# Optimization experiments

Hardware: AMD Instinct MI355X
Metric: run time of the kernel (lower is better)

## Reference

```python
import jax, jax.numpy as jnp
import numpy as np
import math

B, N, NDIM = 8, 8192, 2
WIDTH, HEADS, OUT_C, LATENT_D = 128, 4, 128, 128
N_POINT, N_SAMPLE, RADIUS, PATCH = 128, 8, 0.2, 8
MAX_DEG = 15
POS_DIM = NDIM * (1 + 2 * MAX_DEG)  # 62
SELF_LAYERS = 3


def setup_inputs() -> dict:
    ks = jax.random.split(jax.random.key(0), 16)
    f32 = jnp.float32
    def nrm(k, shape, s=0.02):
        return jax.random.normal(k, shape, dtype=f32) * s
    W = WIDTH
    inp = {
        'points': jax.random.uniform(ks[0], (B, N, NDIM), dtype=f32),
        'pe_w': nrm(ks[1], (POS_DIM, W)), 'pe_b': jnp.zeros((W,), f32),
        'conv1_w': nrm(ks[2], (W, W + NDIM, PATCH, 1)), 'conv1_b': jnp.zeros((W,), f32),
        'conv2_w': nrm(ks[3], (W, W, PATCH, 1)), 'conv2_b': jnp.zeros((W,), f32),
        'output_tokens': jax.random.normal(ks[4], (LATENT_D, W), dtype=f32),
        'ln_pre_s': jnp.ones((W,), f32), 'ln_pre_b': jnp.zeros((W,), f32),
        'c_ln1_s': jnp.ones((W,), f32), 'c_ln1_b': jnp.zeros((W,), f32),
        'c_ln2_s': jnp.ones((W,), f32), 'c_ln2_b': jnp.zeros((W,), f32),
        'c_q_w': nrm(ks[5], (W, W)), 'c_q_b': jnp.zeros((W,), f32),
        'c_kv_w': nrm(ks[6], (W, 2 * W)), 'c_kv_b': jnp.zeros((2 * W,), f32),
        'c_proj_w': nrm(ks[7], (W, W)), 'c_proj_b': jnp.zeros((W,), f32),
        'c_ln3_s': jnp.ones((W,), f32), 'c_ln3_b': jnp.zeros((W,), f32),
        'c_mlp1_w': nrm(ks[8], (W, 4 * W)), 'c_mlp1_b': jnp.zeros((4 * W,), f32),
        'c_mlp2_w': nrm(ks[9], (4 * W, W)), 'c_mlp2_b': jnp.zeros((W,), f32),
        's_ln1_s': jnp.ones((SELF_LAYERS, W), f32), 's_ln1_b': jnp.zeros((SELF_LAYERS, W), f32),
        's_qkv_w': nrm(ks[10], (SELF_LAYERS, W, 3 * W)), 's_qkv_b': jnp.zeros((SELF_LAYERS, 3 * W), f32),
        's_proj_w': nrm(ks[11], (SELF_LAYERS, W, W)), 's_proj_b': jnp.zeros((SELF_LAYERS, W), f32),
        's_ln2_s': jnp.ones((SELF_LAYERS, W), f32), 's_ln2_b': jnp.zeros((SELF_LAYERS, W), f32),
        's_mlp1_w': nrm(ks[12], (SELF_LAYERS, W, 4 * W)), 's_mlp1_b': jnp.zeros((SELF_LAYERS, 4 * W), f32),
        's_mlp2_w': nrm(ks[13], (SELF_LAYERS, 4 * W, W)), 's_mlp2_b': jnp.zeros((SELF_LAYERS, W), f32),
        'ln_post_s': jnp.ones((W,), f32), 'ln_post_b': jnp.zeros((W,), f32),
        'out_w': nrm(ks[14], (W, OUT_C)), 'out_b': jnp.zeros((OUT_C,), f32),
    }
    return inp


def _layer_norm(x, s, b):
    m = jnp.mean(x, -1, keepdims=True)
    v = jnp.mean(jnp.square(x - m), -1, keepdims=True)
    return (x - m) * jax.lax.rsqrt(v + 1e-5) * s + b


def _posenc_nerf(x):
    # point-e nerf posenc: concat([x, sin(xb), sin(xb + pi/2)])
    scales = 2.0 ** jnp.arange(MAX_DEG, dtype=jnp.float32)
    xb = (x[..., None, :] * scales[:, None]).reshape(*x.shape[:-1], -1)
    emb = jnp.sin(jnp.concatenate([xb, xb + 0.5 * jnp.pi], axis=-1))
    return jnp.concatenate([x, emb], axis=-1)  # [..., C*(1+2*MAX_DEG)]


def _mha(q, k, v):
    b, tq, w = q.shape
    dh = w // HEADS
    qh = q.reshape(b, tq, HEADS, dh)
    kh = k.reshape(b, -1, HEADS, dh)
    vh = v.reshape(b, -1, HEADS, dh)
    scores = jnp.einsum('bqhd,bkhd->bhqk', qh, kh) * (1.0 / math.sqrt(dh))
    attn = jax.nn.softmax(scores, axis=-1)
    return jnp.einsum('bhqk,bkhd->bqhd', attn, vh).reshape(b, tq, w)


def _circ_conv(x, w, b):
    # Conv2d kernel (PATCH,1), stride 1, circular padding (PATCH//2, 0)
    p = PATCH // 2
    xp = jnp.concatenate([x[:, :, -p:], x, x[:, :, :p]], axis=2)
    y = jax.lax.conv_general_dilated(xp, w, (1, 1), 'VALID',
                                     dimension_numbers=('NCHW', 'OIHW', 'NCHW'))
    return y + b[None, :, None, None]


def _forward(points, pe_w, pe_b, conv1_w, conv1_b, conv2_w, conv2_b, output_tokens,
             ln_pre_s, ln_pre_b, c_ln1_s, c_ln1_b, c_ln2_s, c_ln2_b, c_q_w, c_q_b,
             c_kv_w, c_kv_b, c_proj_w, c_proj_b, c_ln3_s, c_ln3_b, c_mlp1_w, c_mlp1_b,
             c_mlp2_w, c_mlp2_b, s_ln1_s, s_ln1_b, s_qkv_w, s_qkv_b, s_proj_w, s_proj_b,
             s_ln2_s, s_ln2_b, s_mlp1_w, s_mlp1_b, s_mlp2_w, s_mlp2_b, ln_post_s, ln_post_b,
             out_w, out_b):
    bsz, n, _ = points.shape
    dataset_emb = _posenc_nerf(points) @ pe_w + pe_b             # [B,N,W]
    # ---- PointSetEmbedding (fps_method='first' -> first n_point centers) ----
    new_xyz = points[:, :N_POINT]                                # [B,S,2]
    sqr = jnp.sum(jnp.square(new_xyz[:, :, None] - points[:, None]), -1)  # [B,S,N]
    base = jnp.broadcast_to(jnp.arange(n, dtype=jnp.int32), sqr.shape)
    idx = jnp.where(sqr > RADIUS ** 2, n, base)
    idx = jnp.sort(idx, axis=-1)[:, :, :N_SAMPLE]
    idx = jnp.where(idx == n, idx[:, :, :1], idx)                # [B,S,K] ball-query indices
    gather = jax.vmap(lambda a, i: a[i])
    grouped_xyz = gather(points, idx) - new_xyz[:, :, None]      # [B,S,K,2] relative coords
    grouped_pts = gather(dataset_emb, idx)                       # [B,S,K,W]
    feats = jnp.concatenate([grouped_xyz, grouped_pts], -1)      # [B,S,K,W+2]
    x = jnp.transpose(feats, (0, 3, 2, 1))                       # [B,C,K,S]
    x = jax.nn.silu(_circ_conv(x, conv1_w, conv1_b))
    x = jax.nn.silu(_circ_conv(x, conv2_w, conv2_b))
    data_tokens = jnp.transpose(x.mean(axis=2), (0, 2, 1))       # [B,S,W]
    # ---- Perceiver: cross-attn then self-attn ----
    lat = jnp.broadcast_to(output_tokens[None], (bsz, LATENT_D, WIDTH))
    h = _layer_norm(jnp.concatenate([data_tokens, lat], axis=1), ln_pre_s, ln_pre_b)
    q = _layer_norm(h, c_ln1_s, c_ln1_b) @ c_q_w + c_q_b
    kv = _layer_norm(dataset_emb, c_ln2_s, c_ln2_b) @ c_kv_w + c_kv_b
    k, v = jnp.split(kv, 2, axis=-1)
    h = h + (_mha(q, k, v) @ c_proj_w + c_proj_b)
    t = _layer_norm(h, c_ln3_s, c_ln3_b)
    h = h + (jax.nn.gelu(t @ c_mlp1_w + c_mlp1_b, approximate=False) @ c_mlp2_w + c_mlp2_b)
    for i in range(SELF_LAYERS):
        qkv = _layer_norm(h, s_ln1_s[i], s_ln1_b[i]) @ s_qkv_w[i] + s_qkv_b[i]
        q, k, v = jnp.split(qkv, 3, axis=-1)
        h = h + (_mha(q, k, v) @ s_proj_w[i] + s_proj_b[i])
        t = _layer_norm(h, s_ln2_s[i], s_ln2_b[i])
        h = h + (jax.nn.gelu(t @ s_mlp1_w[i] + s_mlp1_b[i], approximate=False) @ s_mlp2_w[i] + s_mlp2_b[i])
    h = h[:, -LATENT_D:]
    return jnp.tanh(_layer_norm(h, ln_post_s, ln_post_b) @ out_w + out_b)


def reference(points, pe_w, pe_b, conv1_w, conv1_b, conv2_w, conv2_b, output_tokens,
              ln_pre_s, ln_pre_b, c_ln1_s, c_ln1_b, c_ln2_s, c_ln2_b, c_q_w, c_q_b,
              c_kv_w, c_kv_b, c_proj_w, c_proj_b, c_ln3_s, c_ln3_b, c_mlp1_w, c_mlp1_b,
              c_mlp2_w, c_mlp2_b, s_ln1_s, s_ln1_b, s_qkv_w, s_qkv_b, s_proj_w, s_proj_b,
              s_ln2_s, s_ln2_b, s_mlp1_w, s_mlp1_b, s_mlp2_w, s_mlp2_b, ln_post_s, ln_post_b,
              out_w, out_b):
    return _forward(points, pe_w, pe_b, conv1_w, conv1_b, conv2_w, conv2_b, output_tokens,
                    ln_pre_s, ln_pre_b, c_ln1_s, c_ln1_b, c_ln2_s, c_ln2_b, c_q_w, c_q_b,
                    c_kv_w, c_kv_b, c_proj_w, c_proj_b, c_ln3_s, c_ln3_b, c_mlp1_w, c_mlp1_b,
                    c_mlp2_w, c_mlp2_b, s_ln1_s, s_ln1_b, s_qkv_w, s_qkv_b, s_proj_w, s_proj_b,
                    s_ln2_s, s_ln2_b, s_mlp1_w, s_mlp1_b, s_mlp2_w, s_mlp2_b, ln_post_s, ln_post_b,
                    out_w, out_b)
```

## Files before the change

### kernel.cpp

```cpp
#include <hip/hip_runtime.h>
#include <math.h>


namespace {

constexpr int NP = 8192;
constexpr int WD = 128;
constexpr int POSD = 62;
constexpr float R2C = 0.04f;
constexpr float QSCALE = 0.17677669529663687f;
constexpr float HALFPI = 1.5707963705062866f;

typedef __bf16 bf16x8 __attribute__((ext_vector_type(8)));
typedef float f32x4 __attribute__((ext_vector_type(4)));
union U16B { uint4 u; bf16x8 h; unsigned short s[8]; };

__device__ __forceinline__ float b2f(unsigned short u) {
  unsigned v = (unsigned)u << 16;
  return __builtin_bit_cast(float, v);
}

constexpr size_t AO_WQ     = 0;
constexpr size_t AO_WKV    = 16384;
constexpr size_t AO_WPROJC = 49152;
// ... 66 lines not shown
    const float* __restrict__ w1, const float* __restrict__ w2,
    unsigned short* __restrict__ dst) {
  const size_t i = (size_t)blockIdx.x * 256 + threadIdx.x;
  if (i >= AO_TOT) return;
  float v;
  if (i < AO_WKV) {
    size_t j = i;            v = wq[(j & 127) * 128 + (j >> 7)];
  } else if (i < AO_WPROJC) {
    size_t j = i - AO_WKV;   v = wkv[(j & 127) * 256 + (j >> 7)];
  } else if (i < AO_WMLP1C) {
    size_t j = i - AO_WPROJC; v = wprojc[(j & 127) * 128 + (j >> 7)];
  } else if (i < AO_WMLP2C) {
    size_t j = i - AO_WMLP1C; v = wmlp1c[(j & 127) * 512 + (j >> 7)];
  } else if (i < AO_WQKVS) {
    size_t j = i - AO_WMLP2C; v = wmlp2c[(j & 511) * 128 + (j >> 9)];
  } else if (i < AO_WPROJS) {
    size_t j = i - AO_WQKVS;
    size_t L = j / 49152, jj = j % 49152;
    v = wqkvs[L * 49152 + (jj & 127) * 384 + (jj >> 7)];
  } else if (i < AO_WMLP1S) {
    size_t j = i - AO_WPROJS;
    size_t L = j / 16384, jj = j % 16384;
    v = wprojs[L * 16384 + (jj & 127) * 128 + (jj >> 7)];
  } else if (i < AO_WMLP2S) {
    size_t j = i - AO_WMLP1S;
    size_t L = j / 65536, jj = j % 65536;
    v = wmlp1s[L * 65536 + (jj & 127) * 512 + (jj >> 7)];
  } else if (i < AO_WOUT) {
    size_t j = i - AO_WMLP2S;
    size_t L = j / 65536, jj = j % 65536;
    v = wmlp2s[L * 65536 + (jj & 511) * 128 + (jj >> 9)];
  } else if (i < AO_W1B) {
    size_t j = i - AO_WOUT;  v = wout[(j & 127) * 128 + (j >> 7)];
  } else if (i < AO_W2B) {
    size_t j = i - AO_W1B;
    size_t c = j / 1056, k = j % 1056;
    v = (k < 1040) ? w1[c * 1040 + k] : 0.f;
  } else {
    size_t j = i - AO_W2B;   v = w2[(j >> 10) * 1024 + (j & 1023)];
  }
  __bf16 bv = (__bf16)v;
  dst[i] = *(unsigned short*)&bv;
}

__global__ __launch_bounds__(256) void k_kvgc(
    const unsigned short* __restrict__ embb,
    const unsigned short* __restrict__ wkvt,
    const float* __restrict__ kvbias, unsigned short* __restrict__ kb,
    unsigned short* __restrict__ vb, const float* __restrict__ lnS,
    const float* __restrict__ lnB, const float* __restrict__ pts,
    const unsigned short* __restrict__ w1b, const float* __restrict__ b1,
    const unsigned short* __restrict__ w2b, const float* __restrict__ b2,
    float* __restrict__ dtok) {
  __shared__ __align__(16) char shl[45568];
  __shared__ int sid[2][8];
  const int bx = blockIdx.x;
  const int tid = threadIdx.x;
  const int w = tid >> 6, lane = tid & 63;
  const int l15 = lane & 15, l16 = lane >> 4;

  if (bx >= 512) {
    const int kx = bx - 512;
    const int row0 = (kx & 2047) * 32;
    const int nblk = kx >> 11;
    unsigned short (*Ab)[136] = (unsigned short(*)[136])shl;
    unsigned short (*Bt)[136] = (unsigned short(*)[136])(shl + 8704);
    {
      const int n = tid >> 1, hf = tid & 1;
      const unsigned short* src =
          wkvt + ((size_t)(nblk * 128 + n) * 128 + hf * 64);
#pragma unroll
      for (int q8 = 0; q8 < 8; ++q8)
        *(uint4*)&Bt[n][hf * 64 + q8 * 8] = *(const uint4*)(src + q8 * 8);
    }
    {
      const int r = tid >> 3, seg = tid & 7;
      const unsigned short* ap = embb + (size_t)(row0 + r) * WD + seg * 16;
      U16B w0, w1u;
      w0.u = *(const uint4*)ap;
      w1u.u = *(const uint4*)(ap + 8);
      float xv[16];
#pragma unroll
      for (int j = 0; j < 8; ++j) {
        xv[j] = b2f(w0.s[j]);
        xv[8 + j] = b2f(w1u.s[j]);
      }
      float s = 0.f, sq = 0.f;
#pragma unroll
      for (int j = 0; j < 16; ++j) { s += xv[j]; sq += xv[j] * xv[j]; }
      s += __shfl_xor(s, 1);  sq += __shfl_xor(sq, 1);
      s += __shfl_xor(s, 2);  sq += __shfl_xor(sq, 2);
      s += __shfl_xor(s, 4);  sq += __shfl_xor(sq, 4);
      const float m = s * (1.f / 128.f);
      const float var = fmaxf(sq * (1.f / 128.f) - m * m, 0.f);
      const float rinv = 1.0f / sqrtf(var + 1e-5f);
      U16B u0, u1;
#pragma unroll
      for (int j = 0; j < 16; ++j) {
        int col = seg * 16 + j;
        float y = (xv[j] - m) * rinv * lnS[col] + lnB[col];
        if (j < 8) u0.h[j] = (__bf16)y; else u1.h[j - 8] = (__bf16)y;
      }
      *(uint4*)&Ab[r][seg * 16] = u0.u;
      *(uint4*)&Ab[r][seg * 16 + 8] = u1.u;
    }
    __syncthreads();
    const int rt = w >> 1, ch = w & 1;
    f32x4 acc[4];
#pragma unroll
    for (int j = 0; j < 4; ++j) acc[j] = (f32x4){0.f, 0.f, 0.f, 0.f};
#pragma unroll
    for (int kk = 0; kk < 4; ++kk) {
      U16B ua;
      ua.u = *(const uint4*)&Ab[rt * 16 + l15][kk * 32 + l16 * 8];
#pragma unroll
      for (int ct4 = 0; ct4 < 4; ++ct4) {
        U16B ub;
        ub.u = *(const uint4*)&Bt[(ch * 4 + ct4) * 16 + l15][kk * 32 + l16 * 8];
        acc[ct4] = __builtin_amdgcn_mfma_f32_16x16x32_bf16(ua.h, ub.h,
                                                           acc[ct4], 0, 0, 0);
      }
    }
    unsigned short* Dp = (nblk == 1) ? vb : kb;
#pragma unroll
    for (int ct4 = 0; ct4 < 4; ++ct4) {
      int colL = (ch * 4 + ct4) * 16 + l15;
      float bv = kvbias[nblk * 128 + colL];
#pragma unroll
      for (int r = 0; r < 4; ++r) {
        int row = row0 + rt * 16 + l16 * 4 + r;
        __bf16 ov = (__bf16)(acc[ct4][r] + bv);
        Dp[(size_t)row * 128 + colL] = *(unsigned short*)&ov;
      }
    }
    return;
  }

  const int blk = bx;
  const int b = blk >> 6;
  const int i0 = (blk & 63) * 2;
  unsigned short* ftp  = (unsigned short*)shl;
  unsigned short* Bt1p = (unsigned short*)(shl + 4224);
  unsigned short* y1p  = (unsigned short*)shl;
  unsigned short* Bt2p = (unsigned short*)(shl + 12288);

  if (w < 2) {
    const int i = i0 + w;
    const float cx = pts[((size_t)b * NP + i) * 2];
    const float cy = pts[((size_t)b * NP + i) * 2 + 1];
    int cnt = 0;
    for (int j0 = 0; j0 < NP; j0 += 64) {
      int j = j0 + lane;
      float dx = pts[((size_t)b * NP + j) * 2] - cx;
      float dy = pts[((size_t)b * NP + j) * 2 + 1] - cy;
      float d2 = __fadd_rn(__fmul_rn(dx, dx), __fmul_rn(dy, dy));
      bool ok = !(d2 > R2C);
      unsigned long long m = __ballot(ok);
      int ord = cnt + __popcll(m & ((1ull << lane) - 1ull));
      if (ok && ord < 8) sid[w][ord] = j;
      cnt += (int)__popcll(m);
      if (cnt >= 8) break;
    }
    if (lane < 8 && lane >= cnt) sid[w][lane] = sid[w][0];
  }
  __syncthreads();
  {
    const int pr = tid >> 4, c8 = tid & 15;
    const int spx = pr >> 3, s = pr & 7;
    U16B u;
    u.u = *(const uint4*)(embb + ((size_t)b * NP + sid[spx][s]) * WD + c8 * 8);
#pragma unroll
    for (int j = 0; j < 8; ++j)
      ftp[((size_t)spx * 132 + 2 + c8 * 8 + j) * 8 + s] = u.s[j];
  }
  if (tid < 32) {
    int spx = tid >> 4, s = (tid >> 1) & 7, d = tid & 1;
    float dv = pts[((size_t)b * NP + sid[spx][s]) * 2 + d] -
               pts[((size_t)b * NP + i0 + spx) * 2 + d];
    __bf16 bv = (__bf16)dv;
    ftp[((size_t)spx * 132 + d) * 8 + s] = *(unsigned short*)&bv;
  }
  __syncthreads();
  {
    const int n = tid >> 4, g = tid & 15;
    const int pt = n >> 3, h = n & 7;
#pragma unroll
    for (int it = 0; it < 9; ++it) {
      int cin = g + it * 16;
      if (cin < 130) {
        U16B u0;
        u0.u = *(const uint4*)&ftp[((size_t)pt * 132 + cin) * 8];
        U16B u;
#pragma unroll
        for (int p = 0; p < 8; ++p) u.s[p] = u0.s[(h + p + 4) & 7];
        *(uint4*)&Bt1p[n * 1064 + cin * 8] = u.u;
      } else if (cin < 132) {
        uint4 z; z.x = z.y = z.z = z.w = 0;
        *(uint4*)&Bt1p[n * 1064 + cin * 8] = z;
      }
    }
  }
  __syncthreads();
  f32x4 acc1[2];
  acc1[0] = (f32x4){0.f, 0.f, 0.f, 0.f};
  acc1[1] = (f32x4){0.f, 0.f, 0.f, 0.f};
  {
    const unsigned short* w1r = w1b + (size_t)(w * 32 + l15) * 1056;
#pragma unroll 3
    for (int ks = 0; ks < 33; ++ks) {
      const int k0 = ks * 32 + l16 * 8;
      U16B a0, a1, bb;
      a0.u = *(const uint4*)(w1r + k0);
      a1.u = *(const uint4*)(w1r + 16 * 1056 + k0);
      bb.u = *(const uint4*)&Bt1p[l15 * 1064 + k0];
      acc1[0] = __builtin_amdgcn_mfma_f32_16x16x32_bf16(a0.h, bb.h, acc1[0],
                                                        0, 0, 0);
      acc1[1] = __builtin_amdgcn_mfma_f32_16x16x32_bf16(a1.h, bb.h, acc1[1],
                                                        0, 0, 0);
    }
  }
  __syncthreads();
  {
    const int pt = l15 >> 3, h = l15 & 7;
#pragma unroll
    for (int t = 0; t < 2; ++t)
#pragma unroll
      for (int r = 0; r < 4; ++r) {
        int c = w * 32 + t * 16 + l16 * 4 + r;
        float x = acc1[t][r] + b1[c];
        float sy = x / (1.f + __expf(-x));
        __bf16 bh = (__bf16)sy;
        unsigned short bits = *(unsigned short*)&bh;
        size_t yb = ((size_t)pt * 128 + c) * 24;
        y1p[yb + h] = bits;
        if (h == 0) y1p[yb + 8] = bits;
      }
  }
  f32x4 acc2[2][2];
#pragma unroll
  for (int t = 0; t < 2; ++t)
#pragma unroll
    for (int nt = 0; nt < 2; ++nt) acc2[t][nt] = (f32x4){0.f, 0.f, 0.f, 0.f};
  for (int hf = 0; hf < 2; ++hf) {
    __syncthreads();
    {
      const int n2 = tid >> 3, g = tid & 7;
      const int pt = n2 / 9, h2 = n2 % 9;
#pragma unroll
      for (int it = 0; it < 8; ++it) {
        int c1loc = g + it * 8;
        if (n2 < 18) {
          int c1 = hf * 64 + c1loc;
          size_t yb = ((size_t)pt * 128 + c1) * 24;
          U16B u0;
          u0.u = *(const uint4*)&y1p[yb];
          unsigned short yv[9];
#pragma unroll
          for (int j = 0; j < 8; ++j) yv[j] = u0.s[j];
          yv[8] = y1p[yb + 8];
          U16B o;
#pragma unroll
          for (int p = 0; p < 8; ++p) o.s[p] = yv[(h2 + p + 5) % 9];
          *(uint4*)&Bt2p[n2 * 520 + c1loc * 8] = o.u;
        } else {
          uint4 z; z.x = z.y = z.z = z.w = 0;
          *(uint4*)&Bt2p[n2 * 520 + c1loc * 8] = z;
        }
      }
    }
    __syncthreads();
    const unsigned short* w2r = w2b + (size_t)(w * 32 + l15) * 1024 + hf * 512;
#pragma unroll 4
    for (int ks = 0; ks < 16; ++ks) {
      const int k0 = ks * 32 + l16 * 8;
      U16B a0, a1, b0, b1u;
      a0.u = *(const uint4*)(w2r + k0);
      a1.u = *(const uint4*)(w2r + 16 * 1024 + k0);
      b0.u = *(const uint4*)&Bt2p[l15 * 520 + k0];
      b1u.u = *(const uint4*)&Bt2p[(16 + l15) * 520 + k0];
      acc2[0][0] = __builtin_amdgcn_mfma_f32_16x16x32_bf16(a0.h, b0.h,
                                                           acc2[0][0], 0, 0, 0);
      acc2[0][1] = __builtin_amdgcn_mfma_f32_16x16x32_bf16(a0.h, b1u.h,
                                                           acc2[0][1], 0, 0, 0);
      acc2[1][0] = __builtin_amdgcn_mfma_f32_16x16x32_bf16(a1.h, b0.h,
                                                           acc2[1][0], 0, 0, 0);
      acc2[1][1] = __builtin_amdgcn_mfma_f32_16x16x32_bf16(a1.h, b1u.h,
                                                           acc2[1][1], 0, 0, 0);
    }
  }
  float s0[2][4], s1[2][4];
#pragma unroll
  for (int t = 0; t < 2; ++t)
#pragma unroll
    for (int r = 0; r < 4; ++r) { s0[t][r] = 0.f; s1[t][r] = 0.f; }
#pragma unroll
  for (int t = 0; t < 2; ++t)
#pragma unroll
    for (int nt = 0; nt < 2; ++nt) {
      const int n2 = nt * 16 + l15;
      if (n2 < 18) {
        const float wgt = (n2 % 9 == 0) ? 2.f : 1.f;
#pragma unroll
        for (int r = 0; r < 4; ++r) {
          int c = w * 32 + t * 16 + l16 * 4 + r;
          float x = acc2[t][nt][r] + b2[c];
          float sv = wgt * (x / (1.f + __expf(-x)));
          if (n2 < 9) s0[t][r] += sv; else s1[t][r] += sv;
        }
      }
    }
#pragma unroll
  for (int t = 0; t < 2; ++t)
#pragma unroll
    for (int r = 0; r < 4; ++r) {
      float a = s0[t][r], bq = s1[t][r];
      a += __shfl_xor(a, 1);  bq += __shfl_xor(bq, 1);
      a += __shfl_xor(a, 2);  bq += __shfl_xor(bq, 2);
      a += __shfl_xor(a, 4);  bq += __shfl_xor(bq, 4);
      a += __shfl_xor(a, 8);  bq += __shfl_xor(bq, 8);
      if (l15 == 0) {
        int c = w * 32 + t * 16 + l16 * 4 + r;
        dtok[((size_t)b * 128 + i0) * WD + c] = a / 10.0f;
        dtok[((size_t)b * 128 + i0 + 1) * WD + c] = bq / 10.0f;
      }
    }
}

__global__ __launch_bounds__(64) void k_concat_ln(
    const float* __restrict__ dtok, const float* __restrict__ otok,
    const float* __restrict__ g, const float* __restrict__ bta,
    float* __restrict__ h0) {
  const int row = blockIdx.x;
  const int b = row >> 8, t = row & 255;
  const int lane = threadIdx.x;
  const float* src = (t < 128) ? (dtok + ((size_t)b * 128 + t) * WD)
                               : (otok + (size_t)(t - 128) * WD);
  const float2 x2 = *(const float2*)(src + lane * 2);
  float s = x2.x + x2.y;
  float sq = x2.x * x2.x + x2.y * x2.y;
#pragma unroll
  for (int o = 1; o < 64; o <<= 1) {
    s += __shfl_xor(s, o);
    sq += __shfl_xor(sq, o);
  }
  float m = s * (1.f / 128.f);
  float var = fmaxf(sq * (1.f / 128.f) - m * m, 0.f);
  float r = 1.0f / sqrtf(var + 1e-5f);
  int c = lane * 2;
  float2 o2;
  o2.x = (x2.x - m) * r * g[c] + bta[c];
  o2.y = (x2.y - m) * r * g[c + 1] + bta[c + 1];
  *(float2*)(h0 + (size_t)row * WD + c) = o2;
}

template <int ABF, int OBF>
__global__ __launch_bounds__(256) void k_bgemm16(
    const void* __restrict__ A, int lda, const unsigned short* __restrict__ wt,
    const float* __restrict__ bias, const float* __restrict__ res, int ldres,
    void* __restrict__ D, int ldd, int K, int act,
    const float* __restrict__ lnS, const float* __restrict__ lnB, int keep,
    int skip, float oscale, int scaleCols) {
  __shared__ unsigned short Ab[16][136];
  __shared__ unsigned short Bt[64][136];
  const int tid = threadIdx.x;
  const int row0 = blockIdx.x * 16;
  const int col0 = blockIdx.y * 64;
  const int w = tid >> 6, lane = tid & 63;
  const int l15 = lane & 15, l16 = lane >> 4;
  f32x4 acc = (f32x4){0.f, 0.f, 0.f, 0.f};
  for (int kt = 0; kt < K; kt += 128) {
    if (kt) __syncthreads();
    {
      const int n = tid >> 2, q = tid & 3;
      const unsigned short* src = wt + (size_t)(col0 + n) * K + kt + q * 32;
      *(uint4*)&Bt[n][q * 32] = *(const uint4*)src;
      *(uint4*)&Bt[n][q * 32 + 8] = *(const uint4*)(src + 8);
      *(uint4*)&Bt[n][q * 32 + 16] = *(const uint4*)(src + 16);
      *(uint4*)&Bt[n][q * 32 + 24] = *(const uint4*)(src + 24);
    }
    {
      const int r = tid >> 4, seg = tid & 15;
      const int grow = row0 + r;
      const int srow = (grow / keep) * (keep + skip) + skip + grow % keep;
      if (ABF) {
        const unsigned short* ap =
            (const unsigned short*)A + (size_t)srow * lda + kt + seg * 8;
        *(uint4*)&Ab[r][seg * 8] = *(const uint4*)ap;
      } else {
        const float* ap = (const float*)A + (size_t)srow * lda + kt + seg * 8;
        float4 v0 = *(const float4*)ap;
        float4 v1 = *(const float4*)(ap + 4);
        float xv[8] = {v0.x, v0.y, v0.z, v0.w, v1.x, v1.y, v1.z, v1.w};
        if (lnS != nullptr) {
          float s = 0.f, sq = 0.f;
#pragma unroll
          for (int j = 0; j < 8; ++j) { s += xv[j]; sq += xv[j] * xv[j]; }
          s += __shfl_xor(s, 1);  sq += __shfl_xor(sq, 1);
          s += __shfl_xor(s, 2);  sq += __shfl_xor(sq, 2);
          s += __shfl_xor(s, 4);  sq += __shfl_xor(sq, 4);
          s += __shfl_xor(s, 8);  sq += __shfl_xor(sq, 8);
          const float m = s * (1.f / 128.f);
          const float var = fmaxf(sq * (1.f / 128.f) - m * m, 0.f);
          const float rinv = 1.0f / sqrtf(var + 1e-5f);
#pragma unroll
          for (int j = 0; j < 8; ++j) {
            int col = seg * 8 + j;
            xv[j] = (xv[j] - m) * rinv * lnS[col] + lnB[col];
          }
        }
        U16B u0;
#pragma unroll
        for (int j = 0; j < 8; ++j) u0.h[j] = (__bf16)xv[j];
        *(uint4*)&Ab[r][seg * 8] = u0.u;
      }
    }
    __syncthreads();
#pragma unroll
    for (int kk = 0; kk < 4; ++kk) {
      U16B ua, ub;
      ua.u = *(const uint4*)&Ab[l15][kk * 32 + l16 * 8];
      ub.u = *(const uint4*)&Bt[w * 16 + l15][kk * 32 + l16 * 8];
      acc = __builtin_amdgcn_mfma_f32_16x16x32_bf16(ua.h, ub.h, acc, 0, 0, 0);
    }
  }
  {
    const int colL = w * 16 + l15;
    const int col = col0 + colL;
    const float bv = bias[col];
#pragma unroll
    for (int r = 0; r < 4; ++r) {
      const int row = row0 + l16 * 4 + r;
      float x = acc[r] + bv;
      if (col0 < scaleCols) x *= oscale;
      if (act == 1) x = 0.5f * x * (1.0f + erff(x * 0.7071067811865476f));
      else if (act == 2) x = tanhf(x);
      if (res != nullptr) x += res[(size_t)row * ldres + col];
      if (OBF) {
        __bf16 ov = (__bf16)x;
        ((unsigned short*)D)[(size_t)row * ldd + col] = *(unsigned short*)&ov;
      } else {
        ((float*)D)[(size_t)row * ldd + col] = x;
// ... 77 lines not shown
      }

#pragma unroll
    for (int m = 0; m < 4; ++m) {
      const f32x4 zf = {0.f, 0.f, 0.f, 0.f};
      f32x4 sf[4];
#pragma unroll
      for (int ksb = 0; ksb < 4; ++ksb)
        sf[ksb] = __builtin_amdgcn_mfma_f32_16x16x32_bf16(qf[m], kf[ksb], zf,
                                                          0, 0, 0);
#pragma unroll
      for (int ksb = 0; ksb < 4; ++ksb)
#pragma unroll
        for (int r = 0; r < 4; ++r) {
          float p = __expf(sf[ksb][r]);
          __bf16 pb = (__bf16)p;
          Pl[w][(l16 * 4 + r) * 72 + ksb * 16 + l15] = *(unsigned short*)&pb;
        }
      asm volatile("s_waitcnt lgkmcnt(0)" ::: "memory");
      bf16x8 pa[2];
#pragma unroll
      for (int kc = 0; kc < 2; ++kc) {
        U16B u;
        u.u = *(const uint4*)&Pl[w][l15 * 72 + kc * 32 + l16 * 8];
        pa[kc] = u.h;
      }
      lsum[m] = __builtin_amdgcn_mfma_f32_16x16x32_bf16(pa[0], ones, lsum[m],
                                                        0, 0, 0);
      lsum[m] = __builtin_amdgcn_mfma_f32_16x16x32_bf16(pa[1], ones, lsum[m],
                                                        0, 0, 0);
#pragma unroll
      for (int kc = 0; kc < 2; ++kc)
#pragma unroll
        for (int d = 0; d < 2; ++d)
          o[m][d] = __builtin_amdgcn_mfma_f32_16x16x32_bf16(pa[kc], vf[kc][d],
                                                            o[m][d], 0, 0, 0);
    }
  }

  const size_t ob = (size_t)bx * 8192;
#pragma unroll
  for (int m = 0; m < 4; ++m) {
    int qrow = w * 64 + m * 16 + l16 * 4;
#pragma unroll
    for (int r = 0; r < 4; ++r) {
#pragma unroll
      for (int d = 0; d < 2; ++d) {
        __bf16 bo = (__bf16)o[m][d][r];
        opart[ob + (qrow + r) * 32 + d * 16 + l15] = *(unsigned short*)&bo;
      }
      if (l15 == 0) lbuf[(size_t)bx * 256 + qrow + r] = lsum[m][r];
    }
  }
}

__global__ __launch_bounds__(256) void k_attn_comb(
    const unsigned short* __restrict__ opart, const float* __restrict__ lbuf,
    float* __restrict__ O, int S) {
  const int bx = blockIdx.x;
  const int qt = bx & 7, h = (bx >> 3) & 3, b = bx >> 5;
  const int tid = threadIdx.x;
  const int qq = tid >> 3, g = tid & 7;
  const int q = qt * 32 + qq;
  const int pb = (b * 4 + h) * S;
  float L = 0.f;
  float4 o4 = make_float4(0.f, 0.f, 0.f, 0.f);
  for (int s = 0; s < S; ++s) {
    L += lbuf[(size_t)(pb + s) * 256 + q];
    uint2 p2 = *(const uint2*)(opart + (size_t)(pb + s) * 8192 + q * 32 + g * 4);
    unsigned short* ps = (unsigned short*)&p2;
    o4.x += b2f(ps[0]);
    o4.y += b2f(ps[1]);
    o4.z += b2f(ps[2]);
    o4.w += b2f(ps[3]);
  }
  float inv = 1.f / L;
  size_t orow = (size_t)(b * 256 + q);
  float4 res = make_float4(o4.x * inv, o4.y * inv, o4.z * inv, o4.w * inv);
  *(float4*)(O + orow * WD + h * 32 + g * 4) = res;
}

}

extern "C" void kernel_launch(void* const* d_in, const int* in_sizes, int n_in,
                              void* d_out, int out_size, void* d_ws,
                              size_t ws_size, hipStream_t stream) {
  const float* pts      = (const float*)d_in[0];
  const float* pe_w     = (const float*)d_in[1];
  const float* pe_b     = (const float*)d_in[2];
  const float* conv1_w  = (const float*)d_in[3];
  const float* conv1_b  = (const float*)d_in[4];
  const float* conv2_w  = (const float*)d_in[5];
  const float* conv2_b  = (const float*)d_in[6];
  const float* otok     = (const float*)d_in[7];
  const float* ln_pre_s = (const float*)d_in[8];
  const float* ln_pre_b = (const float*)d_in[9];
  const float* c_ln1_s  = (const float*)d_in[10];
  const float* c_ln1_b  = (const float*)d_in[11];
  const float* c_ln2_s  = (const float*)d_in[12];
  const float* c_ln2_b  = (const float*)d_in[13];
  const float* c_q_w    = (const float*)d_in[14];
  const float* c_q_b    = (const float*)d_in[15];
  const float* c_kv_w   = (const float*)d_in[16];
  const float* c_kv_b   = (const float*)d_in[17];
  const float* c_proj_w = (const float*)d_in[18];
  const float* c_proj_b = (const float*)d_in[19];
  const float* c_ln3_s  = (const float*)d_in[20];
  const float* c_ln3_b  = (const float*)d_in[21];
  const float* c_mlp1_w = (const float*)d_in[22];
  const float* c_mlp1_b = (const float*)d_in[23];
  const float* c_mlp2_w = (const float*)d_in[24];
  const float* c_mlp2_b = (const float*)d_in[25];
  const float* s_ln1_s  = (const float*)d_in[26];
  const float* s_ln1_b  = (const float*)d_in[27];
  const float* s_qkv_w  = (const float*)d_in[28];
  const float* s_qkv_b  = (const float*)d_in[29];
  const float* s_proj_w = (const float*)d_in[30];
  const float* s_proj_b = (const float*)d_in[31];
  const float* s_ln2_s  = (const float*)d_in[32];
  const float* s_ln2_b  = (const float*)d_in[33];
  const float* s_mlp1_w = (const float*)d_in[34];
  const float* s_mlp1_b = (const float*)d_in[35];
  const float* s_mlp2_w = (const float*)d_in[36];
  const float* s_mlp2_b = (const float*)d_in[37];
  const float* lnpost_s = (const float*)d_in[38];
  const float* lnpost_b = (const float*)d_in[39];
  const float* out_w    = (const float*)d_in[40];
  const float* out_b    = (const float*)d_in[41];

  char* ws = (char*)d_ws;
  constexpr size_t MB = 1024 * 1024;
  unsigned short* embb = (unsigned short*)(ws);
  unsigned short* kbuf = (unsigned short*)(ws + 32 * MB);
  unsigned short* vbuf = (unsigned short*)(ws + 48 * MB);
  char*  b3   = ws + 64 * MB;
  float* dtok = (float*)(b3);
  float* hbuf = (float*)(b3 + 524288);
  unsigned short* qbuf = (unsigned short*)(b3 + 524288 + 1048576);
  float* att  = (float*)(b3 + 524288 + 2097152);
  unsigned short* mid = (unsigned short*)(b3 + 524288 + 3145728);
  unsigned short* qkv = (unsigned short*)(b3 + 524288 + 7340032);
  unsigned short* arena = (unsigned short*)(b3 + 524288 + 10485760);
  unsigned short* opart = (unsigned short*)(ws);
  float* lbuf  = (float*)(b3 + 16 * MB);

  const int IDK = 1 << 28;

  k_prep<<<(int)((AO_TOT + 255) / 256), 256, 0, stream>>>(
      c_q_w, c_kv_w, c_proj_w, c_mlp1_w, c_mlp2_w, s_qkv_w, s_proj_w,
      s_mlp1_w, s_mlp2_w, out_w, conv1_w, conv2_w, arena);
  k_posenc<<<2048, 256, 0, stream>>>(pts, pe_w, pe_b, embb);
  k_kvgc<<<4608, 256, 0, stream>>>(embb, arena + AO_WKV, c_kv_b, kbuf, vbuf,
                                   c_ln2_s, c_ln2_b, pts, arena + AO_W1B,
                                   conv1_b, arena + AO_W2B, conv2_b, dtok);
  k_concat_ln<<<2048, 64, 0, stream>>>(dtok, otok, ln_pre_s, ln_pre_b, hbuf);
  k_bgemm16<0, 1><<<dim3(128, 2), 256, 0, stream>>>(
      hbuf, 128, arena + AO_WQ, c_q_b, nullptr, 0, qbuf, 128, 128, 0, c_ln1_s,
      c_ln1_b, IDK, 0, QSCALE, 128);
  k_attn_mfma<<<1024, 256, 0, stream>>>(qbuf, 128, kbuf, 128, vbuf, 128,
                                        opart, lbuf, 8192, 32, 256);
  k_attn_comb<<<256, 256, 0, stream>>>(opart, lbuf, att, 32);
  k_bgemm16<0, 0><<<dim3(128, 2), 256, 0, stream>>>(
      att, 128, arena + AO_WPROJC, c_proj_b, hbuf, 128, hbuf, 128, 128, 0,
      nullptr, nullptr, IDK, 0, 1.f, 0);
  k_bgemm16<0, 1><<<dim3(128, 8), 256, 0, stream>>>(
      hbuf, 128, arena + AO_WMLP1C, c_mlp1_b, nullptr, 0, mid, 512, 128, 1,
      c_ln3_s, c_ln3_b, IDK, 0, 1.f, 0);
  k_bgemm16<1, 0><<<dim3(128, 2), 256, 0, stream>>>(
      mid, 512, arena + AO_WMLP2C, c_mlp2_b, hbuf, 128, hbuf, 128, 512, 0,
      nullptr, nullptr, IDK, 0, 1.f, 0);
  for (int i = 0; i < 3; ++i) {
    k_bgemm16<0, 1><<<dim3(128, 6), 256, 0, stream>>>(
        hbuf, 128, arena + AO_WQKVS + (size_t)i * 49152, s_qkv_b + i * 384,
        nullptr, 0, qkv, 384, 128, 0, s_ln1_s + i * 128, s_ln1_b + i * 128,
        IDK, 0, QSCALE, 128);
    k_attn_mfma<<<128, 256, 0, stream>>>(qkv, 384, qkv + 128, 384, qkv + 256,
                                         384, opart, lbuf, 256, 4, 64);
    k_attn_comb<<<256, 256, 0, stream>>>(opart, lbuf, att, 4);
    k_bgemm16<0, 0><<<dim3(128, 2), 256, 0, stream>>>(
        att, 128, arena + AO_WPROJS + (size_t)i * 16384, s_proj_b + i * 128,
        hbuf, 128, hbuf, 128, 128, 0, nullptr, nullptr, IDK, 0, 1.f, 0);
    k_bgemm16<0, 1><<<dim3(128, 8), 256, 0, stream>>>(
        hbuf, 128, arena + AO_WMLP1S + (size_t)i * 65536, s_mlp1_b + i * 512,
        nullptr, 0, mid, 512, 128, 1, s_ln2_s + i * 128, s_ln2_b + i * 128,
        IDK, 0, 1.f, 0);
    k_bgemm16<1, 0><<<dim3(128, 2), 256, 0, stream>>>(
        mid, 512, arena + AO_WMLP2S + (size_t)i * 65536, s_mlp2_b + i * 128,
        hbuf, 128, hbuf, 128, 512, 0, nullptr, nullptr, IDK, 0, 1.f, 0);
  }
  k_bgemm16<0, 0><<<dim3(64, 2), 256, 0, stream>>>(
      hbuf, 128, arena + AO_WOUT, out_b, nullptr, 0, (float*)d_out, 128, 128,
      2, lnpost_s, lnpost_b, 128, 128, 1.f, 0);
}
```

Before: 246.6 us.

## Process four patches per conv block and fuse attention combine into proj GEMM

The grouping/conv part of k_kvgc now handles four center points per block instead of two. This halves the block count and gives each MFMA A-fragment two or three B tiles. The conv1 and conv2 stages are staged through smaller shared-memory tiles in multiple passes, and the final sum moves to an LDS buffer plus a per-column loop. Separately, the attention combine kernel is removed and its split-softmax reduction is folded into the A-tile load of the projection GEMM, which drops four launches and the fp32 att round trip. The risk is that the fused combine is recomputed for each of the two N-column blocks, and the conv path adds extra syncs.

Result: faster. 236.8 us (-4.0%).

```diff
diff --git a/kernel.cpp b/kernel.cpp
--- a/kernel.cpp
+++ b/kernel.cpp
@@ -142,15 +142,15 @@
     const unsigned short* __restrict__ w1b, const float* __restrict__ b1,
     const unsigned short* __restrict__ w2b, const float* __restrict__ b2,
     float* __restrict__ dtok) {
-  __shared__ __align__(16) char shl[45568];
-  __shared__ int sid[2][8];
+  __shared__ __align__(16) char shl[43776];
+  __shared__ int sid[4][8];
   const int bx = blockIdx.x;
   const int tid = threadIdx.x;
   const int w = tid >> 6, lane = tid & 63;
   const int l15 = lane & 15, l16 = lane >> 4;
 
-  if (bx >= 512) {
-    const int kx = bx - 512;
+  if (bx >= 256) {
+    const int kx = bx - 256;
     const int row0 = (kx & 2047) * 32;
     const int nblk = kx >> 11;
     unsigned short (*Ab)[136] = (unsigned short(*)[136])shl;
@@ -226,15 +226,15 @@
     return;
   }
 
-  const int blk = bx;
-  const int b = blk >> 6;
-  const int i0 = (blk & 63) * 2;
+  const int b = bx >> 5;
+  const int i0 = (bx & 31) * 4;
   unsigned short* ftp  = (unsigned short*)shl;
-  unsigned short* Bt1p = (unsigned short*)(shl + 4224);
+  unsigned short* Bt1p = (unsigned short*)(shl + 8448);
   unsigned short* y1p  = (unsigned short*)shl;
-  unsigned short* Bt2p = (unsigned short*)(shl + 12288);
-
-  if (w < 2) {
+  unsigned short* Bt2p = (unsigned short*)(shl + 16384);
+  float* tmpp = (float*)(shl + 16384);
+
+  {
     const int i = i0 + w;
     const float cx = pts[((size_t)b * NP + i) * 2];
     const float cy = pts[((size_t)b * NP + i) * 2 + 1];
@@ -255,165 +255,187 @@
   }
   __syncthreads();
   {
-    const int pr = tid >> 4, c8 = tid & 15;
-    const int spx = pr >> 3, s = pr & 7;
-    U16B u;
-    u.u = *(const uint4*)(embb + ((size_t)b * NP + sid[spx][s]) * WD + c8 * 8);
-#pragma unroll
-    for (int j = 0; j < 8; ++j)
-      ftp[((size_t)spx * 132 + 2 + c8 * 8 + j) * 8 + s] = u.s[j];
-  }
-  if (tid < 32) {
-    int spx = tid >> 4, s = (tid >> 1) & 7, d = tid & 1;
-    float dv = pts[((size_t)b * NP + sid[spx][s]) * 2 + d] -
-               pts[((size_t)b * NP + i0 + spx) * 2 + d];
+    const int pr = tid >> 3, c16 = tid & 7;
+    const int pt = pr >> 3, s = pr & 7;
+    const unsigned short* src =
+        embb + ((size_t)b * NP + sid[pt][s]) * WD + c16 * 16;
+    U16B u0, u1;
+    u0.u = *(const uint4*)src;
+    u1.u = *(const uint4*)(src + 8);
+#pragma unroll
+    for (int j = 0; j < 8; ++j) {
+      ftp[((size_t)pt * 132 + 2 + c16 * 16 + j) * 8 + s] = u0.s[j];
+      ftp[((size_t)pt * 132 + 2 + c16 * 16 + 8 + j) * 8 + s] = u1.s[j];
+    }
+  }
+  if (tid < 64) {
+    int pt = tid >> 4, rem = tid & 15;
+    int s = rem >> 1, d = rem & 1;
+    float dv = pts[((size_t)b * NP + sid[pt][s]) * 2 + d] -
+               pts[((size_t)b * NP + i0 + pt) * 2 + d];
     __bf16 bv = (__bf16)dv;
-    ftp[((size_t)spx * 132 + d) * 8 + s] = *(unsigned short*)&bv;
+    ftp[((size_t)pt * 132 + d) * 8 + s] = *(unsigned short*)&bv;
+    int pt2 = tid >> 4, cin2 = 130 + ((tid >> 3) & 1), s2 = tid & 7;
+    ftp[((size_t)pt2 * 132 + cin2) * 8 + s2] = 0;
+  }
+  __syncthreads();
+  f32x4 acc1[2][2];
+#pragma unroll
+  for (int t = 0; t < 2; ++t)
+#pragma unroll
+    for (int bt = 0; bt < 2; ++bt) acc1[t][bt] = (f32x4){0.f, 0.f, 0.f, 0.f};
+  for (int ps = 0; ps < 2; ++ps) {
+    const int cinbase = ps ? 68 : 0;
+    const int CW = ps ? 64 : 68;
+    if (ps) __syncthreads();
+    {
+      const int n = tid >> 3, g = tid & 7;
+      const int pt = n >> 3, h = n & 7;
+#pragma unroll
+      for (int it = 0; it < 9; ++it) {
+        int cl = g + it * 8;
+        if (cl < CW) {
+          int cin = cinbase + cl;
+          U16B u0, u;
+          u0.u = *(const uint4*)&ftp[((size_t)pt * 132 + cin) * 8];
+#pragma unroll
+          for (int p = 0; p < 8; ++p) u.s[p] = u0.s[(h + p + 4) & 7];
+          *(uint4*)&Bt1p[n * 552 + cl * 8] = u.u;
+        }
+      }
+    }
+    __syncthreads();
+    const unsigned short* w1r =
+        w1b + (size_t)(w * 32 + l15) * 1056 + cinbase * 8;
+    const int kit = ps ? 16 : 17;
+    for (int ks = 0; ks < kit; ++ks) {
+      const int k0 = ks * 32 + l16 * 8;
+      U16B a0, a1, b0, b1u;
+      a0.u = *(const uint4*)(w1r + k0);
+      a1.u = *(const uint4*)(w1r + 16 * 1056 + k0);
+      b0.u = *(const uint4*)&Bt1p[l15 * 552 + k0];
+      b1u.u = *(const uint4*)&Bt1p[(16 + l15) * 552 + k0];
+      acc1[0][0] = __builtin_amdgcn_mfma_f32_16x16x32_bf16(a0.h, b0.h,
+                                                           acc1[0][0], 0, 0, 0);
+      acc1[0][1] = __builtin_amdgcn_mfma_f32_16x16x32_bf16(a0.h, b1u.h,
+                                                           acc1[0][1], 0, 0, 0);
+      acc1[1][0] = __builtin_amdgcn_mfma_f32_16x16x32_bf16(a1.h, b0.h,
+                                                           acc1[1][0], 0, 0, 0);
+      acc1[1][1] = __builtin_amdgcn_mfma_f32_16x16x32_bf16(a1.h, b1u.h,
+                                                           acc1[1][1], 0, 0, 0);
+    }
   }
   __syncthreads();
   {
-    const int n = tid >> 4, g = tid & 15;
-    const int pt = n >> 3, h = n & 7;
-#pragma unroll
-    for (int it = 0; it < 9; ++it) {
-      int cin = g + it * 16;
-      if (cin < 130) {
-        U16B u0;
-        u0.u = *(const uint4*)&ftp[((size_t)pt * 132 + cin) * 8];
-        U16B u;
-#pragma unroll
-        for (int p = 0; p < 8; ++p) u.s[p] = u0.s[(h + p + 4) & 7];
-        *(uint4*)&Bt1p[n * 1064 + cin * 8] = u.u;
-      } else if (cin < 132) {
-        uint4 z; z.x = z.y = z.z = z.w = 0;
-        *(uint4*)&Bt1p[n * 1064 + cin * 8] = z;
-      }
-    }
-  }
-  __syncthreads();
-  f32x4 acc1[2];
-  acc1[0] = (f32x4){0.f, 0.f, 0.f, 0.f};
-  acc1[1] = (f32x4){0.f, 0.f, 0.f, 0.f};
-  {
-    const unsigned short* w1r = w1b + (size_t)(w * 32 + l15) * 1056;
-#pragma unroll 3
-    for (int ks = 0; ks < 33; ++ks) {
-      const int k0 = ks * 32 + l16 * 8;
-      U16B a0, a1, bb;
-      a0.u = *(const uint4*)(w1r + k0);
-      a1.u = *(const uint4*)(w1r + 16 * 1056 + k0);
-      bb.u = *(const uint4*)&Bt1p[l15 * 1064 + k0];
-      acc1[0] = __builtin_amdgcn_mfma_f32_16x16x32_bf16(a0.h, bb.h, acc1[0],
-                                                        0, 0, 0);
-      acc1[1] = __builtin_amdgcn_mfma_f32_16x16x32_bf16(a1.h, bb.h, acc1[1],
-                                                        0, 0, 0);
-    }
-  }
-  __syncthreads();
-  {
-    const int pt = l15 >> 3, h = l15 & 7;
 #pragma unroll
     for (int t = 0; t < 2; ++t)
 #pragma unroll
-      for (int r = 0; r < 4; ++r) {
-        int c = w * 32 + t * 16 + l16 * 4 + r;
-        float x = acc1[t][r] + b1[c];
-        float sy = x / (1.f + __expf(-x));
-        __bf16 bh = (__bf16)sy;
-        unsigned short bits = *(unsigned short*)&bh;
-        size_t yb = ((size_t)pt * 128 + c) * 24;
-        y1p[yb + h] = bits;
-        if (h == 0) y1p[yb + 8] = bits;
-      }
-  }
-  f32x4 acc2[2][2];
+      for (int bt = 0; bt < 2; ++bt) {
+        const int n = bt * 16 + l15;
+        const int pt = n >> 3, h = n & 7;
+#pragma unroll
+        for (int r = 0; r < 4; ++r) {
+          int c = w * 32 + t * 16 + l16 * 4 + r;
+          float x = acc1[t][bt][r] + b1[c];
+          float sy = x / (1.f + __expf(-x));
+          __bf16 bh = (__bf16)sy;
+          unsigned short bits = *(unsigned short*)&bh;
+          size_t yb = ((size_t)pt * 128 + c) * 16;
+          y1p[yb + h] = bits;
+          if (h == 0) y1p[yb + 8] = bits;
+        }
+      }
+  }
+  f32x4 acc2[2][3];
 #pragma unroll
   for (int t = 0; t < 2; ++t)
 #pragma unroll
-    for (int nt = 0; nt < 2; ++nt) acc2[t][nt] = (f32x4){0.f, 0.f, 0.f, 0.f};
-  for (int hf = 0; hf < 2; ++hf) {
+    for (int bt = 0; bt < 3; ++bt) acc2[t][bt] = (f32x4){0.f, 0.f, 0.f, 0.f};
+  for (int ps = 0; ps < 4; ++ps) {
     __syncthreads();
     {
-      const int n2 = tid >> 3, g = tid & 7;
-      const int pt = n2 / 9, h2 = n2 % 9;
-#pragma unroll
-      for (int it = 0; it < 8; ++it) {
-        int c1loc = g + it * 8;
-        if (n2 < 18) {
-          int c1 = hf * 64 + c1loc;
-          size_t yb = ((size_t)pt * 128 + c1) * 24;
-          U16B u0;
-          u0.u = *(const uint4*)&y1p[yb];
-          unsigned short yv[9];
-#pragma unroll
-          for (int j = 0; j < 8; ++j) yv[j] = u0.s[j];
-          yv[8] = y1p[yb + 8];
+      const int g = tid & 7;
+      for (int n2 = tid >> 3; n2 < 38; n2 += 32) {
+        const int pt = n2 / 9, h2 = n2 % 9;
+#pragma unroll
+        for (int it = 0; it < 4; ++it) {
+          int cl = g + it * 8;
           U16B o;
-#pragma unroll
-          for (int p = 0; p < 8; ++p) o.s[p] = yv[(h2 + p + 5) % 9];
-          *(uint4*)&Bt2p[n2 * 520 + c1loc * 8] = o.u;
-        } else {
-          uint4 z; z.x = z.y = z.z = z.w = 0;
-          *(uint4*)&Bt2p[n2 * 520 + c1loc * 8] = z;
+          if (n2 < 36) {
+            int c1 = ps * 32 + cl;
+            size_t yb = ((size_t)pt * 128 + c1) * 16;
+            U16B u0;
+            u0.u = *(const uint4*)&y1p[yb];
+            unsigned short yv[9];
+#pragma unroll
+            for (int j = 0; j < 8; ++j) yv[j] = u0.s[j];
+            yv[8] = y1p[yb + 8];
+#pragma unroll
+            for (int p = 0; p < 8; ++p) o.s[p] = yv[(h2 + p + 5) % 9];
+          } else {
+            o.u.x = o.u.y = o.u.z = o.u.w = 0;
+          }
+          *(uint4*)&Bt2p[n2 * 264 + cl * 8] = o.u;
         }
       }
     }
     __syncthreads();
-    const unsigned short* w2r = w2b + (size_t)(w * 32 + l15) * 1024 + hf * 512;
-#pragma unroll 4
-    for (int ks = 0; ks < 16; ++ks) {
+    const unsigned short* w2r =
+        w2b + (size_t)(w * 32 + l15) * 1024 + ps * 256;
+    int r2 = 32 + l15;
+    if (r2 > 37) r2 = 37;
+#pragma unroll
+    for (int ks = 0; ks < 8; ++ks) {
       const int k0 = ks * 32 + l16 * 8;
-      U16B a0, a1, b0, b1u;
+      U16B a0, a1, b0, b1u, b2u;
       a0.u = *(const uint4*)(w2r + k0);
       a1.u = *(const uint4*)(w2r + 16 * 1024 + k0);
-      b0.u = *(const uint4*)&Bt2p[l15 * 520 + k0];
-      b1u.u = *(const uint4*)&Bt2p[(16 + l15) * 520 + k0];
+      b0.u = *(const uint4*)&Bt2p[l15 * 264 + k0];
+      b1u.u = *(const uint4*)&Bt2p[(16 + l15) * 264 + k0];
+      b2u.u = *(const uint4*)&Bt2p[r2 * 264 + k0];
       acc2[0][0] = __builtin_amdgcn_mfma_f32_16x16x32_bf16(a0.h, b0.h,
                                                            acc2[0][0], 0, 0, 0);
       acc2[0][1] = __builtin_amdgcn_mfma_f32_16x16x32_bf16(a0.h, b1u.h,
                                                            acc2[0][1], 0, 0, 0);
+      acc2[0][2] = __builtin_amdgcn_mfma_f32_16x16x32_bf16(a0.h, b2u.h,
+                                                           acc2[0][2], 0, 0, 0);
       acc2[1][0] = __builtin_amdgcn_mfma_f32_16x16x32_bf16(a1.h, b0.h,
                                                            acc2[1][0], 0, 0, 0);
       acc2[1][1] = __builtin_amdgcn_mfma_f32_16x16x32_bf16(a1.h, b1u.h,
                                                            acc2[1][1], 0, 0, 0);
-    }
-  }
-  float s0[2][4], s1[2][4];
-#pragma unroll
-  for (int t = 0; t < 2; ++t)
-#pragma unroll
-    for (int r = 0; r < 4; ++r) { s0[t][r] = 0.f; s1[t][r] = 0.f; }
-#pragma unroll
-  for (int t = 0; t < 2; ++t)
-#pragma unroll
-    for (int nt = 0; nt < 2; ++nt) {
-      const int n2 = nt * 16 + l15;
-      if (n2 < 18) {
-        const float wgt = (n2 % 9 == 0) ? 2.f : 1.f;
-#pragma unroll
-        for (int r = 0; r < 4; ++r) {
-          int c = w * 32 + t * 16 + l16 * 4 + r;
-          float x = acc2[t][nt][r] + b2[c];
-          float sv = wgt * (x / (1.f + __expf(-x)));
-          if (n2 < 9) s0[t][r] += sv; else s1[t][r] += sv;
+      acc2[1][2] = __builtin_amdgcn_mfma_f32_16x16x32_bf16(a1.h, b2u.h,
+                                                           acc2[1][2], 0, 0, 0);
+    }
+  }
+  __syncthreads();
+  {
+#pragma unroll
+    for (int t = 0; t < 2; ++t)
+#pragma unroll
+      for (int bt = 0; bt < 3; ++bt) {
+        const int n2 = bt * 16 + l15;
+        if (n2 < 36) {
+          const int h2 = n2 % 9;
+          const float wgt = (h2 == 0) ? 2.f : 1.f;
+#pragma unroll
+          for (int r = 0; r < 4; ++r) {
+            int c = w * 32 + t * 16 + l16 * 4 + r;
+            float x = acc2[t][bt][r] + b2[c];
+            tmpp[n2 * 132 + c] = wgt * (x / (1.f + __expf(-x)));
+          }
         }
       }
-    }
-#pragma unroll
-  for (int t = 0; t < 2; ++t)
-#pragma unroll
-    for (int r = 0; r < 4; ++r) {
-      float a = s0[t][r], bq = s1[t][r];
-      a += __shfl_xor(a, 1);  bq += __shfl_xor(bq, 1);
-      a += __shfl_xor(a, 2);  bq += __shfl_xor(bq, 2);
-      a += __shfl_xor(a, 4);  bq += __shfl_xor(bq, 4);
-      a += __shfl_xor(a, 8);  bq += __shfl_xor(bq, 8);
-      if (l15 == 0) {
-        int c = w * 32 + t * 16 + l16 * 4 + r;
-        dtok[((size_t)b * 128 + i0) * WD + c] = a / 10.0f;
-        dtok[((size_t)b * 128 + i0 + 1) * WD + c] = bq / 10.0f;
-      }
-    }
+  }
+  __syncthreads();
+#pragma unroll
+  for (int k = 0; k < 2; ++k) {
+    int idx = tid + k * 256;
+    int pt = idx >> 7, c = idx & 127;
+    float ssum = 0.f;
+#pragma unroll
+    for (int h2 = 0; h2 < 9; ++h2) ssum += tmpp[(pt * 9 + h2) * 132 + c];
+    dtok[((size_t)b * 128 + i0 + pt) * WD + c] = ssum / 10.0f;
+  }
 }
 
 __global__ __launch_bounds__(64) void k_concat_ln(
@@ -443,13 +465,15 @@
   *(float2*)(h0 + (size_t)row * WD + c) = o2;
 }
 
-template <int ABF, int OBF>
+template <int ABF, int OBF, int COMB>
 __global__ __launch_bounds__(256) void k_bgemm16(
     const void* __restrict__ A, int lda, const unsigned short* __restrict__ wt,
     const float* __restrict__ bias, const float* __restrict__ res, int ldres,
     void* __restrict__ D, int ldd, int K, int act,
     const float* __restrict__ lnS, const float* __restrict__ lnB, int keep,
-    int skip, float oscale, int scaleCols) {
+    int skip, float oscale, int scaleCols,
+    const unsigned short* __restrict__ opart, const float* __restrict__ lbuf,
+    int S) {
   __shared__ unsigned short Ab[16][136];
   __shared__ unsigned short Bt[64][136];
   const int tid = threadIdx.x;
@@ -471,12 +495,31 @@
     {
       const int r = tid >> 4, seg = tid & 15;
       const int grow = row0 + r;
-      const int srow = (grow / keep) * (keep + skip) + skip + grow % keep;
-      if (ABF) {
+      if (COMB) {
+        const int bq = grow >> 8, q = grow & 255;
+        const int h = seg >> 2, d0 = (seg & 3) * 8;
+        const int pb = (bq * 4 + h) * S;
+        float L = 0.f;
+        float vals[8] = {0.f, 0.f, 0.f, 0.f, 0.f, 0.f, 0.f, 0.f};
+        for (int s = 0; s < S; ++s) {
+          L += lbuf[(size_t)(pb + s) * 256 + q];
+          uint4 p4 = *(const uint4*)(opart + (size_t)(pb + s) * 8192 + q * 32 + d0);
+          const unsigned short* ps = (const unsigned short*)&p4;
+#pragma unroll
+          for (int j = 0; j < 8; ++j) vals[j] += b2f(ps[j]);
+        }
+        const float inv = 1.0f / L;
+        U16B u0;
+#pragma unroll
+        for (int j = 0; j < 8; ++j) u0.h[j] = (__bf16)(vals[j] * inv);
+        *(uint4*)&Ab[r][seg * 8] = u0.u;
+      } else if (ABF) {
+        const int srow = (grow / keep) * (keep + skip) + skip + grow % keep;
         const unsigned short* ap =
             (const unsigned short*)A + (size_t)srow * lda + kt + seg * 8;
         *(uint4*)&Ab[r][seg * 8] = *(const uint4*)ap;
       } else {
+        const int srow = (grow / keep) * (keep + skip) + skip + grow % keep;
         const float* ap = (const float*)A + (size_t)srow * lda + kt + seg * 8;
         float4 v0 = *(const float4*)ap;
         float4 v1 = *(const float4*)(ap + 4);
@@ -660,32 +703,6 @@
       if (l15 == 0) lbuf[(size_t)bx * 256 + qrow + r] = lsum[m][r];
     }
   }
-}
-
-__global__ __launch_bounds__(256) void k_attn_comb(
-    const unsigned short* __restrict__ opart, const float* __restrict__ lbuf,
-    float* __restrict__ O, int S) {
-  const int bx = blockIdx.x;
-  const int qt = bx & 7, h = (bx >> 3) & 3, b = bx >> 5;
-  const int tid = threadIdx.x;
-  const int qq = tid >> 3, g = tid & 7;
-  const int q = qt * 32 + qq;
-  const int pb = (b * 4 + h) * S;
-  float L = 0.f;
-  float4 o4 = make_float4(0.f, 0.f, 0.f, 0.f);
-  for (int s = 0; s < S; ++s) {
-    L += lbuf[(size_t)(pb + s) * 256 + q];
-    uint2 p2 = *(const uint2*)(opart + (size_t)(pb + s) * 8192 + q * 32 + g * 4);
-    unsigned short* ps = (unsigned short*)&p2;
-    o4.x += b2f(ps[0]);
-    o4.y += b2f(ps[1]);
-    o4.z += b2f(ps[2]);
-    o4.w += b2f(ps[3]);
-  }
-  float inv = 1.f / L;
-  size_t orow = (size_t)(b * 256 + q);
-  float4 res = make_float4(o4.x * inv, o4.y * inv, o4.z * inv, o4.w * inv);
-  *(float4*)(O + orow * WD + h * 32 + g * 4) = res;
 }
 
 }
@@ -745,7 +762,6 @@
   float* dtok = (float*)(b3);
   float* hbuf = (float*)(b3 + 524288);
   unsigned short* qbuf = (unsigned short*)(b3 + 524288 + 1048576);
-  float* att  = (float*)(b3 + 524288 + 2097152);
   unsigned short* mid = (unsigned short*)(b3 + 524288 + 3145728);
   unsigned short* qkv = (unsigned short*)(b3 + 524288 + 7340032);
   unsigned short* arena = (unsigned short*)(b3 + 524288 + 10485760);
@@ -758,45 +774,45 @@
       c_q_w, c_kv_w, c_proj_w, c_mlp1_w, c_mlp2_w, s_qkv_w, s_proj_w,
       s_mlp1_w, s_mlp2_w, out_w, conv1_w, conv2_w, arena);
   k_posenc<<<2048, 256, 0, stream>>>(pts, pe_w, pe_b, embb);
-  k_kvgc<<<4608, 256, 0, stream>>>(embb, arena + AO_WKV, c_kv_b, kbuf, vbuf,
+  k_kvgc<<<4352, 256, 0, stream>>>(embb, arena + AO_WKV, c_kv_b, kbuf, vbuf,
                                    c_ln2_s, c_ln2_b, pts, arena + AO_W1B,
                                    conv1_b, arena + AO_W2B, conv2_b, dtok);
   k_concat_ln<<<2048, 64, 0, stream>>>(dtok, otok, ln_pre_s, ln_pre_b, hbuf);
-  k_bgemm16<0, 1><<<dim3(128, 2), 256, 0, stream>>>(
+  k_bgemm16<0, 1, 0><<<dim3(128, 2), 256, 0, stream>>>(
       hbuf, 128, arena + AO_WQ, c_q_b, nullptr, 0, qbuf, 128, 128, 0, c_ln1_s,
-      c_ln1_b, IDK, 0, QSCALE, 128);
+      c_ln1_b, IDK, 0, QSCALE, 128, nullptr, nullptr, 0);
   k_attn_mfma<<<1024, 256, 0, stream>>>(qbuf, 128, kbuf, 128, vbuf, 128,
                                         opart, lbuf, 8192, 32, 256);
-  k_attn_comb<<<256, 256, 0, stream>>>(opart, lbuf, att, 32);
-  k_bgemm16<0, 0><<<dim3(128, 2), 256, 0, stream>>>(
-      att, 128, arena + AO_WPROJC, c_proj_b, hbuf, 128, hbuf, 128, 128, 0,
-      nullptr, nullptr, IDK, 0, 1.f, 0);
-  k_bgemm16<0, 1><<<dim3(128, 8), 256, 0, stream>>>(
+  k_bgemm16<0, 0, 1><<<dim3(128, 2), 256, 0, stream>>>(
+      nullptr, 128, arena + AO_WPROJC, c_proj_b, hbuf, 128, hbuf, 128, 128, 0,
+      nullptr, nullptr, IDK, 0, 1.f, 0, opart, lbuf, 32);
+  k_bgemm16<0, 1, 0><<<dim3(128, 8), 256, 0, stream>>>(
       hbuf, 128, arena + AO_WMLP1C, c_mlp1_b, nullptr, 0, mid, 512, 128, 1,
-      c_ln3_s, c_ln3_b, IDK, 0, 1.f, 0);
-  k_bgemm16<1, 0><<<dim3(128, 2), 256, 0, stream>>>(
+      c_ln3_s, c_ln3_b, IDK, 0, 1.f, 0, nullptr, nullptr, 0);
+  k_bgemm16<1, 0, 0><<<dim3(128, 2), 256, 0, stream>>>(
       mid, 512, arena + AO_WMLP2C, c_mlp2_b, hbuf, 128, hbuf, 128, 512, 0,
-      nullptr, nullptr, IDK, 0, 1.f, 0);
+      nullptr, nullptr, IDK, 0, 1.f, 0, nullptr, nullptr, 0);
   for (int i = 0; i < 3; ++i) {
-    k_bgemm16<0, 1><<<dim3(128, 6), 256, 0, stream>>>(
+    k_bgemm16<0, 1, 0><<<dim3(128, 6), 256, 0, stream>>>(
         hbuf, 128, arena + AO_WQKVS + (size_t)i * 49152, s_qkv_b + i * 384,
         nullptr, 0, qkv, 384, 128, 0, s_ln1_s + i * 128, s_ln1_b + i * 128,
-        IDK, 0, QSCALE, 128);
+        IDK, 0, QSCALE, 128, nullptr, nullptr, 0);
     k_attn_mfma<<<128, 256, 0, stream>>>(qkv, 384, qkv + 128, 384, qkv + 256,
                                          384, opart, lbuf, 256, 4, 64);
-    k_attn_comb<<<256, 256, 0, stream>>>(opart, lbuf, att, 4);
-    k_bgemm16<0, 0><<<dim3(128, 2), 256, 0, stream>>>(
-        att, 128, arena + AO_WPROJS + (size_t)i * 16384, s_proj_b + i * 128,
-        hbuf, 128, hbuf, 128, 128, 0, nullptr, nullptr, IDK, 0, 1.f, 0);
-    k_bgemm16<0, 1><<<dim3(128, 8), 256, 0, stream>>>(
+    k_bgemm16<0, 0, 1><<<dim3(128, 2), 256, 0, stream>>>(
+        nullptr, 128, arena + AO_WPROJS + (size_t)i * 16384,
+        s_proj_b + i * 128, hbuf, 128, hbuf, 128, 128, 0, nullptr, nullptr,
+        IDK, 0, 1.f, 0, opart, lbuf, 4);
+    k_bgemm16<0, 1, 0><<<dim3(128, 8), 256, 0, stream>>>(
         hbuf, 128, arena + AO_WMLP1S + (size_t)i * 65536, s_mlp1_b + i * 512,
         nullptr, 0, mid, 512, 128, 1, s_ln2_s + i * 128, s_ln2_b + i * 128,
-        IDK, 0, 1.f, 0);
-    k_bgemm16<1, 0><<<dim3(128, 2), 256, 0, stream>>>(
+        IDK, 0, 1.f, 0, nullptr, nullptr, 0);
+    k_bgemm16<1, 0, 0><<<dim3(128, 2), 256, 0, stream>>>(
         mid, 512, arena + AO_WMLP2S + (size_t)i * 65536, s_mlp2_b + i * 128,
-        hbuf, 128, hbuf, 128, 512, 0, nullptr, nullptr, IDK, 0, 1.f, 0);
-  }
-  k_bgemm16<0, 0><<<dim3(64, 2), 256, 0, stream>>>(
+        hbuf, 128, hbuf, 128, 512, 0, nullptr, nullptr, IDK, 0, 1.f, 0,
+        nullptr, nullptr, 0);
+  }
+  k_bgemm16<0, 0, 0><<<dim3(64, 2), 256, 0, stream>>>(
       hbuf, 128, arena + AO_WOUT, out_b, nullptr, 0, (float*)d_out, 128, 128,
-      2, lnpost_s, lnpost_b, 128, 128, 1.f, 0);
+      2, lnpost_s, lnpost_b, 128, 128, 1.f, 0, nullptr, nullptr, 0);
 }
```
